# Kernel optimization log

Measured on AMD Instinct MI355X. Metric: run time of the kernel, lower is better.

The kernel has to match this reference:

```python
import jax, jax.numpy as jnp
import numpy as np

N, E = 8192, 65536
IN_C, OUT_C, EF = 64, 16, 8
L1, L2 = 48, 32  # in - floor((in-out)/3), in - floor(2*(in-out)/3)


def setup_inputs() -> dict:
    key = jax.random.key(0)
    ks = jax.random.split(key, 10)
    rn = lambda k, shape, s: jax.random.normal(k, shape, dtype=jnp.float32) * s
    return {
        "x": jax.random.normal(ks[0], (N, IN_C), dtype=jnp.float32),
        "edge_index": jax.random.randint(ks[1], (2, E), 0, N, dtype=jnp.int32),
        "edge_attr": jax.random.normal(ks[2], (E, EF), dtype=jnp.float32),
        "nn1_w": rn(ks[3], (EF, IN_C * L1), 0.05),
        "nn1_b": jnp.zeros((IN_C * L1,), jnp.float32),
        "root1": rn(ks[4], (IN_C, L1), 0.1),
        "bias1": jnp.zeros((L1,), jnp.float32),
        "nn2_w": rn(ks[5], (EF, L1 * L2), 0.05),
        "nn2_b": jnp.zeros((L1 * L2,), jnp.float32),
        "root2": rn(ks[6], (L1, L2), 0.1),
        "bias2": jnp.zeros((L2,), jnp.float32),
        "mu_w": rn(ks[7], (L2, OUT_C), 0.1),
        "mu_b": jnp.zeros((OUT_C,), jnp.float32),
        "ls_w": rn(ks[8], (L2, OUT_C), 0.1),
        "ls_b": jnp.zeros((OUT_C,), jnp.float32),
    }


def _nnconv(x, src, dst, edge_attr, nn_w, nn_b, root, bias, c_in, c_out):
    # edge MLP -> per-edge weight matrices [E, c_in, c_out]
    w = (edge_attr @ nn_w + nn_b).reshape(-1, c_in, c_out)
    msg = jnp.einsum('ei,eio->eo', x[src], w)  # gather + per-edge matvec
    agg = jax.ops.segment_sum(msg, dst, num_segments=x.shape[0])  # sum aggregation
    return agg + x @ root + bias  # root transform + bias


def _gcn(x, src, dst, w, b):
    n = x.shape[0]
    # degree over target nodes, including self-loop (edge_weight = 1)
    deg = jax.ops.segment_sum(jnp.ones_like(src, jnp.float32), dst, num_segments=n) + 1.0
    dinv = jax.lax.rsqrt(deg)
    h = x @ w
    norm = dinv[src] * dinv[dst]  # [E]
    agg = jax.ops.segment_sum(h[src] * norm[:, None], dst, num_segments=n)
    return agg + h * (1.0 / deg)[:, None] + b  # self-loop contribution: deg_i^{-1}


def reference(x, edge_index, edge_attr, nn1_w, nn1_b, root1, bias1,
              nn2_w, nn2_b, root2, bias2, mu_w, mu_b, ls_w, ls_b):
    src, dst = edge_index[0], edge_index[1]
    h = jax.nn.relu(_nnconv(x, src, dst, edge_attr, nn1_w, nn1_b, root1, bias1, IN_C, L1))
    h = jax.nn.relu(_nnconv(h, src, dst, edge_attr, nn2_w, nn2_b, root2, bias2, L1, L2))
    return (_gcn(h, src, dst, mu_w, mu_b), _gcn(h, src, dst, ls_w, ls_b))
```

## Files before the change

kernel.cpp:

```cpp
#include <hip/hip_runtime.h>

#define NN 8192
#define EE 65536
#define MAXDEG 32
#define ZS1 652
#define ZS2 492
#define WS1 68
#define WS2 100
#define U1_OFF 5216
#define U2_OFF 3936


__global__ __launch_bounds__(256) void k_zero(int* __restrict__ cnt,
                                              int* __restrict__ ssrcb,
                                              float* __restrict__ seab) {
    int n = blockIdx.x * 256 + threadIdx.x;
    cnt[n] = 0;
    ssrcb[n * MAXDEG] = 0;
    float4* p = (float4*)(seab + (size_t)n * MAXDEG * 8);
    p[0] = make_float4(0.f, 0.f, 0.f, 0.f);
    p[1] = make_float4(0.f, 0.f, 0.f, 0.f);
}

__global__ __launch_bounds__(256) void k_bucket(const int* __restrict__ ei,
                                                const float* __restrict__ ea,
                                                const float* __restrict__ nn1_w,
                                                const float* __restrict__ nn1_b,
                                                const float* __restrict__ root1,
                                                const float* __restrict__ nn2_w,
                                                const float* __restrict__ nn2_b,
                                                const float* __restrict__ root2,
                                                int* __restrict__ cnt,
                                                int* __restrict__ ssrcb,
                                                float* __restrict__ seab,
                                                float* __restrict__ WtT1,
                                                float* __restrict__ WtT2) {
    int e = blockIdx.x * 256 + threadIdx.x;
    if (e < 48 * 640) {
        int col = e / 640, k = e - col * 640;
        float v = (k < 512) ? nn1_w[k * 48 + col]
                : (k < 576) ? nn1_b[(k - 512) * 48 + col]
                            : root1[(k - 576) * 48 + col];
        WtT1[e] = v;
    } else if (e < 48 * 640 + 32 * 480) {
        int r = e - 48 * 640;
        int col = r / 480, k = r - col * 480;
        float v = (k < 384) ? nn2_w[k * 32 + col]
                : (k < 432) ? nn2_b[(k - 384) * 32 + col]
                            : root2[(k - 432) * 32 + col];
        WtT2[r] = v;
    }
    if (e >= EE) return;
    int s = ei[e], d = ei[EE + e];
    int pos = atomicAdd(&cnt[d], 1);
    if (pos < MAXDEG) {
        int slot = d * MAXDEG + pos;
        ssrcb[slot] = s;
        const float4* a = (const float4*)(ea + (size_t)e * 8);
        float4* bp = (float4*)(seab + (size_t)slot * 8);
        bp[0] = a[0];
        bp[1] = a[1];
    }
}

__global__ __launch_bounds__(256) void k_L1(const int* __restrict__ cnt,
                                            const int* __restrict__ ssrcb,
                                            const float* __restrict__ seab,
                                            const float* __restrict__ x,
                                            const float* __restrict__ WtT1,
                                            const float* __restrict__ bias1,
                                            float* __restrict__ h1) {
    __shared__ __align__(16) float smem[U1_OFF + 48 * WS1];
    float* Zt = smem;
    float* U  = smem + U1_OFF;
    const int n0 = blockIdx.x * 8;
    {
        const int wv = threadIdx.x >> 6;
        const int i = threadIdx.x & 63;
        const int nnA = wv * 2, nnB = nnA + 1;
        const int rsA = (n0 + nnA) * MAXDEG;
        const int rsB = (n0 + nnB) * MAXDEG;
        float xselfA = x[(size_t)(n0 + nnA) * 64 + i];
        float xselfB = x[(size_t)(n0 + nnB) * 64 + i];
        int dA = cnt[n0 + nnA]; if (dA > MAXDEG) dA = MAXDEG;
        int dB = cnt[n0 + nnB]; if (dB > MAXDEG) dB = MAXDEG;
        const int eA = rsA + dA, eB = rsB + dB;
        int jA = rsA, jB = rsB;
        float aA[8] = {0, 0, 0, 0, 0, 0, 0, 0}, sA = 0.f;
        float aB[8] = {0, 0, 0, 0, 0, 0, 0, 0}, sB = 0.f;
        while (jA < eA || jB < eB) {
            int cjA[8], cjB[8];
#pragma unroll
            for (int p = 0; p < 8; p++) {
                int ja = jA + p; cjA[p] = (ja < eA) ? ja : rsA;
                int jb = jB + p; cjB[p] = (jb < eB) ? jb : rsB;
            }
            int sjA[8], sjB[8];
#pragma unroll
            for (int p = 0; p < 8; p++) { sjA[p] = ssrcb[cjA[p]]; sjB[p] = ssrcb[cjB[p]]; }
            float xvA[8], xvB[8];
#pragma unroll
            for (int p = 0; p < 8; p++) {
                xvA[p] = x[(size_t)sjA[p] * 64 + i];
                xvB[p] = x[(size_t)sjB[p] * 64 + i];
            }
#pragma unroll
            for (int p = 0; p < 8; p++) {
                {
                    const float4* q4 = (const float4*)(seab + (size_t)cjA[p] * 8);
                    float4 e0 = q4[0], e1 = q4[1];
                    float xx = (jA + p < eA) ? xvA[p] : 0.f;
                    aA[0] += e0.x * xx; aA[1] += e0.y * xx; aA[2] += e0.z * xx; aA[3] += e0.w * xx;
                    aA[4] += e1.x * xx; aA[5] += e1.y * xx; aA[6] += e1.z * xx; aA[7] += e1.w * xx;
                    sA += xx;
                }
                {
                    const float4* q4 = (const float4*)(seab + (size_t)cjB[p] * 8);
                    float4 e0 = q4[0], e1 = q4[1];
                    float xx = (jB + p < eB) ? xvB[p] : 0.f;
                    aB[0] += e0.x * xx; aB[1] += e0.y * xx; aB[2] += e0.z * xx; aB[3] += e0.w * xx;
                    aB[4] += e1.x * xx; aB[5] += e1.y * xx; aB[6] += e1.z * xx; aB[7] += e1.w * xx;
                    sB += xx;
                }
            }
            jA += 8; jB += 8;
        }
        float* zrA = Zt + nnA * ZS1;
        float* zrB = Zt + nnB * ZS1;
#pragma unroll
        for (int f = 0; f < 8; f++) { zrA[f * 64 + i] = aA[f]; zrB[f * 64 + i] = aB[f]; }
        zrA[512 + i] = sA; zrB[512 + i] = sB;
        zrA[576 + i] = xselfA;
        zrB[576 + i] = xselfB;
    }
    const int o  = threadIdx.x & 15;
    const int q  = (threadIdx.x >> 4) & 1;
    const int ks = threadIdx.x >> 5;
    const int xsw = (o & 7) << 2;
    const int g0 = threadIdx.x, g1 = threadIdx.x + 256, g2 = threadIdx.x + 512;
    const int c0_ = g0 >> 4, k0_ = (g0 & 15) << 2;
    const int c1_ = g1 >> 4, k1_ = (g1 & 15) << 2;
    const int c2_ = g2 >> 4, k2_ = (g2 & 15) << 2;
    const int sa0 = c0_ * WS1 + (k0_ ^ ((c0_ & 7) << 2));
    const int sa1 = c1_ * WS1 + (k1_ ^ ((c1_ & 7) << 2));
    const int sa2 = c2_ * WS1 + (k2_ ^ ((c2_ & 7) << 2));
    const float* gp0 = WtT1 + c0_ * 640 + k0_;
    const float* gp1 = WtT1 + c1_ * 640 + k1_;
    const float* gp2 = WtT1 + c2_ * 640 + k2_;
    float acc[4][3];
#pragma unroll
    for (int m = 0; m < 4; m++)
#pragma unroll
        for (int cc = 0; cc < 3; cc++) acc[m][cc] = 0.f;
    float4 r0 = *(const float4*)gp0;
    float4 r1 = *(const float4*)gp1;
    float4 r2 = *(const float4*)gp2;
    for (int c = 0; c < 10; ++c) {
        __syncthreads();
        *(float4*)&U[sa0] = r0;
        *(float4*)&U[sa1] = r1;
        *(float4*)&U[sa2] = r2;
        __syncthreads();
        if (c < 9) {
            r0 = *(const float4*)(gp0 + (c + 1) * 64);
            r1 = *(const float4*)(gp1 + (c + 1) * 64);
            r2 = *(const float4*)(gp2 + (c + 1) * 64);
        }
#pragma unroll
        for (int kk = 0; kk < 8; kk += 4) {
            const int kl = ks * 8 + kk;
            const int kx = kl ^ xsw;
            const int kg = c * 64 + kl;
            float4 w0 = *(const float4*)&U[o * WS1 + kx];
            float4 w1 = *(const float4*)&U[(o + 16) * WS1 + kx];
            float4 w2 = *(const float4*)&U[(o + 32) * WS1 + kx];
#pragma unroll
            for (int m = 0; m < 4; m++) {
                float4 z = *(const float4*)&Zt[(q * 4 + m) * ZS1 + kg];
                acc[m][0] += z.x * w0.x; acc[m][1] += z.x * w1.x; acc[m][2] += z.x * w2.x;
                acc[m][0] += z.y * w0.y; acc[m][1] += z.y * w1.y; acc[m][2] += z.y * w2.y;
                acc[m][0] += z.z * w0.z; acc[m][1] += z.z * w1.z; acc[m][2] += z.z * w2.z;
                acc[m][0] += z.w * w0.w; acc[m][1] += z.w * w1.w; acc[m][2] += z.w * w2.w;
            }
        }
    }
    __syncthreads();
#pragma unroll
    for (int m = 0; m < 4; m++) {
        U[(ks * 8 + q * 4 + m) * 48 + o]      = acc[m][0];
        U[(ks * 8 + q * 4 + m) * 48 + o + 16] = acc[m][1];
        U[(ks * 8 + q * 4 + m) * 48 + o + 32] = acc[m][2];
    }
    __syncthreads();
    for (int r = threadIdx.x; r < 8 * 48; r += 256) {
        int nn = r / 48, oc = r - nn * 48;
        float v = bias1[oc];
#pragma unroll
        for (int k = 0; k < 8; k++) v += U[(k * 8 + nn) * 48 + oc];
        h1[(size_t)(n0 + nn) * 48 + oc] = v > 0.f ? v : 0.f;
    }
}

__global__ __launch_bounds__(256) void k_L2(const int* __restrict__ cnt,
                                            const int* __restrict__ ssrcb,
                                            const float* __restrict__ seab,
                                            const float* __restrict__ h1,
                                            const float* __restrict__ WtT2,
                                            const float* __restrict__ bias2,
                                            const float* __restrict__ mu_w,
                                            const float* __restrict__ mu_b,
                                            const float* __restrict__ ls_w,
                                            const float* __restrict__ ls_b,
                                            float* __restrict__ hmu,
                                            float* __restrict__ hls,
                                            float* __restrict__ dinv,
                                            float* __restrict__ out) {
    __shared__ __align__(16) float smem[U2_OFF + 32 * WS2];
    float* Zt = smem;
    float* U  = smem + U2_OFF;
    const int n0 = blockIdx.x * 8;
    {
        const int wv = threadIdx.x >> 6;
        const int i = threadIdx.x & 63;
        if (i < 48) {
            const int nnA = wv * 2, nnB = nnA + 1;
            const int rsA = (n0 + nnA) * MAXDEG;
            const int rsB = (n0 + nnB) * MAXDEG;
            float hselfA = h1[(size_t)(n0 + nnA) * 48 + i];
            float hselfB = h1[(size_t)(n0 + nnB) * 48 + i];
            int dA = cnt[n0 + nnA]; if (dA > MAXDEG) dA = MAXDEG;
            int dB = cnt[n0 + nnB]; if (dB > MAXDEG) dB = MAXDEG;
            const int eA = rsA + dA, eB = rsB + dB;
            int jA = rsA, jB = rsB;
            float aA[8] = {0, 0, 0, 0, 0, 0, 0, 0}, sA = 0.f;
            float aB[8] = {0, 0, 0, 0, 0, 0, 0, 0}, sB = 0.f;
            while (jA < eA || jB < eB) {
                int cjA[8], cjB[8];
#pragma unroll
                for (int p = 0; p < 8; p++) {
                    int ja = jA + p; cjA[p] = (ja < eA) ? ja : rsA;
                    int jb = jB + p; cjB[p] = (jb < eB) ? jb : rsB;
                }
                int sjA[8], sjB[8];
#pragma unroll
                for (int p = 0; p < 8; p++) { sjA[p] = ssrcb[cjA[p]]; sjB[p] = ssrcb[cjB[p]]; }
                float hvA[8], hvB[8];
#pragma unroll
                for (int p = 0; p < 8; p++) {
                    hvA[p] = h1[(size_t)sjA[p] * 48 + i];
                    hvB[p] = h1[(size_t)sjB[p] * 48 + i];
                }
#pragma unroll
                for (int p = 0; p < 8; p++) {
                    {
                        const float4* q4 = (const float4*)(seab + (size_t)cjA[p] * 8);
                        float4 e0 = q4[0], e1 = q4[1];
                        float xx = (jA + p < eA) ? hvA[p] : 0.f;
                        aA[0] += e0.x * xx; aA[1] += e0.y * xx; aA[2] += e0.z * xx; aA[3] += e0.w * xx;
                        aA[4] += e1.x * xx; aA[5] += e1.y * xx; aA[6] += e1.z * xx; aA[7] += e1.w * xx;
                        sA += xx;
                    }
                    {
                        const float4* q4 = (const float4*)(seab + (size_t)cjB[p] * 8);
                        float4 e0 = q4[0], e1 = q4[1];
                        float xx = (jB + p < eB) ? hvB[p] : 0.f;
                        aB[0] += e0.x * xx; aB[1] += e0.y * xx; aB[2] += e0.z * xx; aB[3] += e0.w * xx;
                        aB[4] += e1.x * xx; aB[5] += e1.y * xx; aB[6] += e1.z * xx; aB[7] += e1.w * xx;
                        sB += xx;
                    }
                }
                jA += 8; jB += 8;
            }
            float* zrA = Zt + nnA * ZS2;
            float* zrB = Zt + nnB * ZS2;
#pragma unroll
            for (int f = 0; f < 8; f++) { zrA[f * 48 + i] = aA[f]; zrB[f * 48 + i] = aB[f]; }
            zrA[384 + i] = sA; zrB[384 + i] = sB;
            zrA[432 + i] = hselfA;
            zrB[432 + i] = hselfB;
        }
    }
    const int o  = threadIdx.x & 15;
    const int q  = (threadIdx.x >> 4) & 1;
    const int ks = threadIdx.x >> 5;
    const int xsw = (o & 7) << 2;
    const int g0 = threadIdx.x, g1 = threadIdx.x + 256, g2 = threadIdx.x + 512;
    const int c0_ = g0 / 24, k0_ = (g0 - c0_ * 24) << 2;
    const int c1_ = g1 / 24, k1_ = (g1 - c1_ * 24) << 2;
    const int c2_ = g2 / 24, k2_ = (g2 - c2_ * 24) << 2;
    const int sa0 = c0_ * WS2 + (k0_ ^ ((c0_ & 7) << 2));
    const int sa1 = c1_ * WS2 + (k1_ ^ ((c1_ & 7) << 2));
    const int sa2 = c2_ * WS2 + (k2_ ^ ((c2_ & 7) << 2));
    const float* gp0 = WtT2 + c0_ * 480 + k0_;
    const float* gp1 = WtT2 + c1_ * 480 + k1_;
    const float* gp2 = WtT2 + c2_ * 480 + k2_;
    float acc[4][2];
#pragma unroll
    for (int m = 0; m < 4; m++) { acc[m][0] = 0.f; acc[m][1] = 0.f; }
    float4 r0 = *(const float4*)gp0;
    float4 r1 = *(const float4*)gp1;
    float4 r2 = *(const float4*)gp2;
    for (int c = 0; c < 5; ++c) {
        __syncthreads();
        *(float4*)&U[sa0] = r0;
        *(float4*)&U[sa1] = r1;
        *(float4*)&U[sa2] = r2;
        __syncthreads();
        if (c < 4) {
            r0 = *(const float4*)(gp0 + (c + 1) * 96);
            r1 = *(const float4*)(gp1 + (c + 1) * 96);
            r2 = *(const float4*)(gp2 + (c + 1) * 96);
        }
#pragma unroll
        for (int kk = 0; kk < 12; kk += 4) {
            const int kl = ks * 12 + kk;
            const int kx = kl ^ xsw;
            const int kg = c * 96 + kl;
            float4 w0 = *(const float4*)&U[o * WS2 + kx];
            float4 w1 = *(const float4*)&U[(o + 16) * WS2 + kx];
#pragma unroll
            for (int m = 0; m < 4; m++) {
                float4 z = *(const float4*)&Zt[(q * 4 + m) * ZS2 + kg];
                acc[m][0] += z.x * w0.x; acc[m][1] += z.x * w1.x;
                acc[m][0] += z.y * w0.y; acc[m][1] += z.y * w1.y;
                acc[m][0] += z.z * w0.z; acc[m][1] += z.z * w1.z;
                acc[m][0] += z.w * w0.w; acc[m][1] += z.w * w1.w;
            }
        }
    }
    __syncthreads();
#pragma unroll
    for (int m = 0; m < 4; m++) {
        U[(ks * 8 + q * 4 + m) * 32 + o]      = acc[m][0];
        U[(ks * 8 + q * 4 + m) * 32 + o + 16] = acc[m][1];
    }
    __syncthreads();
    {
        int nn = threadIdx.x >> 5, oc = threadIdx.x & 31;
        float v = bias2[oc];
#pragma unroll
        for (int k = 0; k < 8; k++) v += U[(k * 8 + nn) * 32 + oc];
        U[2048 + nn * 33 + oc] = v > 0.f ? v : 0.f;
    }
    __syncthreads();
    if (threadIdx.x < 128) {
        const int oc = threadIdx.x & 15;
        const int nn = threadIdx.x >> 4;
        const int gn = n0 + nn;
        float am = 0.f, al = 0.f;
#pragma unroll
        for (int i = 0; i < 32; i++) {
            float hv = U[2048 + nn * 33 + i];
            am += hv * mu_w[i * 16 + oc];
            al += hv * ls_w[i * 16 + oc];
        }
        float d = (float)cnt[gn] + 1.0f;
        float di = rsqrtf(d);
        if (oc == 0) dinv[gn] = di;
        hmu[(size_t)gn * 16 + oc] = am;
        hls[(size_t)gn * 16 + oc] = al;
        out[(size_t)gn * 16 + oc] = am / d + mu_b[oc];
        out[(size_t)NN * 16 + (size_t)gn * 16 + oc] = al / d + ls_b[oc];
    }
}

__global__ __launch_bounds__(256) void k_gcn(const int* __restrict__ cnt,
                                             const int* __restrict__ ssrcb,
                                             const float* __restrict__ hmu,
                                             const float* __restrict__ hls,
                                             const float* __restrict__ dinv,
                                             float* __restrict__ out) {
    const int wave = threadIdx.x >> 6;
    const int lane = threadIdx.x & 63;
    const int o = lane & 15, p = lane >> 4;
    const int d = blockIdx.x * 4 + wave;
    int deg = cnt[d]; if (deg > MAXDEG) deg = MAXDEG;
    const int rs = d * MAXDEG, re = rs + deg;
    float am = 0.f, al = 0.f;
    for (int j = rs + p; j < re; j += 8) {
        int jb = j + 4;
        int sa = ssrcb[j];
        int sb = ssrcb[jb < re ? jb : rs];
        float da_ = dinv[sa], db_ = dinv[sb];
        float ma = hmu[(size_t)sa * 16 + o], la = hls[(size_t)sa * 16 + o];
        float mb = hmu[(size_t)sb * 16 + o], lb = hls[(size_t)sb * 16 + o];
        am += ma * da_; al += la * da_;
        if (jb < re) { am += mb * db_; al += lb * db_; }
    }
    am += __shfl_xor(am, 16); al += __shfl_xor(al, 16);
    am += __shfl_xor(am, 32); al += __shfl_xor(al, 32);
    if (p == 0) {
        float dd = dinv[d];
        out[(size_t)d * 16 + o] += am * dd;
        out[(size_t)NN * 16 + (size_t)d * 16 + o] += al * dd;
    }
}

extern "C" void kernel_launch(void* const* d_in, const int* in_sizes, int n_in,
                              void* d_out, int out_size, void* d_ws, size_t ws_size,
                              hipStream_t stream) {
    const float* x     = (const float*)d_in[0];
    const int*   ei    = (const int*)d_in[1];
    const float* ea    = (const float*)d_in[2];
    const float* nn1_w = (const float*)d_in[3];
    const float* nn1_b = (const float*)d_in[4];
    const float* root1 = (const float*)d_in[5];
    const float* bias1 = (const float*)d_in[6];
    const float* nn2_w = (const float*)d_in[7];
    const float* nn2_b = (const float*)d_in[8];
    const float* root2 = (const float*)d_in[9];
    const float* bias2 = (const float*)d_in[10];
    const float* mu_w  = (const float*)d_in[11];
    const float* mu_b  = (const float*)d_in[12];
    const float* ls_w  = (const float*)d_in[13];
    const float* ls_b  = (const float*)d_in[14];
    float* out = (float*)d_out;

    float* W     = (float*)d_ws;
    float* WtT1  = W;
    float* WtT2  = WtT1 + 30720;
    float* seab  = WtT2 + 15360;
    float* h1    = seab + NN * MAXDEG * 8;
    float* hmu   = h1 + 393216;
    float* hls   = hmu + 131072;
    float* dinv  = hls + 131072;
    int* cnt     = (int*)(dinv + 8192);
    int* ssrcb   = cnt + 8192;

    k_zero<<<dim3(NN / 256), dim3(256), 0, stream>>>(cnt, ssrcb, seab);
    k_bucket<<<dim3(EE / 256), dim3(256), 0, stream>>>(ei, ea,
                                                       nn1_w, nn1_b, root1,
                                                       nn2_w, nn2_b, root2,
                                                       cnt, ssrcb, seab, WtT1, WtT2);
    k_L1<<<dim3(NN / 8), dim3(256), 0, stream>>>(cnt, ssrcb, seab, x,
                                                 WtT1, bias1, h1);
    k_L2<<<dim3(NN / 8), dim3(256), 0, stream>>>(cnt, ssrcb, seab, h1,
                                                 WtT2, bias2,
                                                 mu_w, mu_b, ls_w, ls_b,
                                                 hmu, hls, dinv, out);
    k_gcn<<<dim3(NN / 4), dim3(256), 0, stream>>>(cnt, ssrcb,
                                                  hmu, hls, dinv, out);
}
```

Before: 145.5 us.

## Fuse GCN aggregation into layer-2 kernel via push-style atomic scatter

Removes the separate GCN gather kernel. k_bucket now also builds an out-edge bucket list (dstb) with per-source counts. The end of k_L2 then pushes each node's normalized mu/logstd projections to its destinations with float atomicAdd into the output, and k_zero now also clears the output buffer. This drops one launch and the hmu/hls/dinv intermediate round-trip to memory. In exchange it adds many scattered global atomics, an extra atomic per edge during bucketing, and non-deterministic summation order.

```diff
diff --git a/kernel.cpp b/kernel.cpp
--- a/kernel.cpp
+++ b/kernel.cpp
@@ -11,15 +11,22 @@
 #define U2_OFF 3936
 
 
-__global__ __launch_bounds__(256) void k_zero(int* __restrict__ cnt,
+__global__ __launch_bounds__(256) void k_zero(float* __restrict__ out,
+                                              int* __restrict__ cntreg,
                                               int* __restrict__ ssrcb,
                                               float* __restrict__ seab) {
-    int n = blockIdx.x * 256 + threadIdx.x;
-    cnt[n] = 0;
-    ssrcb[n * MAXDEG] = 0;
-    float4* p = (float4*)(seab + (size_t)n * MAXDEG * 8);
-    p[0] = make_float4(0.f, 0.f, 0.f, 0.f);
-    p[1] = make_float4(0.f, 0.f, 0.f, 0.f);
+    int i = blockIdx.x * 256 + threadIdx.x;
+    if (i < 65536) {
+        ((float4*)out)[i] = make_float4(0.f, 0.f, 0.f, 0.f);
+    } else {
+        ((int4*)cntreg)[i - 65536] = make_int4(0, 0, 0, 0);
+    }
+    if (i < NN) {
+        ssrcb[i * MAXDEG] = 0;
+        float4* p = (float4*)(seab + (size_t)i * MAXDEG * 8);
+        p[0] = make_float4(0.f, 0.f, 0.f, 0.f);
+        p[1] = make_float4(0.f, 0.f, 0.f, 0.f);
+    }
 }
 
 __global__ __launch_bounds__(256) void k_bucket(const int* __restrict__ ei,
@@ -31,7 +38,9 @@
                                                 const float* __restrict__ nn2_b,
                                                 const float* __restrict__ root2,
                                                 int* __restrict__ cnt,
+                                                int* __restrict__ cnt_src,
                                                 int* __restrict__ ssrcb,
+                                                int* __restrict__ dstb,
                                                 float* __restrict__ seab,
                                                 float* __restrict__ WtT1,
                                                 float* __restrict__ WtT2) {
@@ -61,6 +70,8 @@
         bp[0] = a[0];
         bp[1] = a[1];
     }
+    int pos2 = atomicAdd(&cnt_src[s], 1);
+    if (pos2 < MAXDEG) dstb[s * MAXDEG + pos2] = d;
 }
 
 __global__ __launch_bounds__(256) void k_L1(const int* __restrict__ cnt,
@@ -202,7 +213,9 @@
 }
 
 __global__ __launch_bounds__(256) void k_L2(const int* __restrict__ cnt,
+                                            const int* __restrict__ cnt_src,
                                             const int* __restrict__ ssrcb,
+                                            const int* __restrict__ dstb,
                                             const float* __restrict__ seab,
                                             const float* __restrict__ h1,
                                             const float* __restrict__ WtT2,
@@ -211,9 +224,6 @@
                                             const float* __restrict__ mu_b,
                                             const float* __restrict__ ls_w,
                                             const float* __restrict__ ls_b,
-                                            float* __restrict__ hmu,
-                                            float* __restrict__ hls,
-                                            float* __restrict__ dinv,
                                             float* __restrict__ out) {
     __shared__ __align__(16) float smem[U2_OFF + 32 * WS2];
     float* Zt = smem;
@@ -356,43 +366,17 @@
         }
         float d = (float)cnt[gn] + 1.0f;
         float di = rsqrtf(d);
-        if (oc == 0) dinv[gn] = di;
-        hmu[(size_t)gn * 16 + oc] = am;
-        hls[(size_t)gn * 16 + oc] = al;
-        out[(size_t)gn * 16 + oc] = am / d + mu_b[oc];
-        out[(size_t)NN * 16 + (size_t)gn * 16 + oc] = al / d + ls_b[oc];
-    }
-}
-
-__global__ __launch_bounds__(256) void k_gcn(const int* __restrict__ cnt,
-                                             const int* __restrict__ ssrcb,
-                                             const float* __restrict__ hmu,
-                                             const float* __restrict__ hls,
-                                             const float* __restrict__ dinv,
-                                             float* __restrict__ out) {
-    const int wave = threadIdx.x >> 6;
-    const int lane = threadIdx.x & 63;
-    const int o = lane & 15, p = lane >> 4;
-    const int d = blockIdx.x * 4 + wave;
-    int deg = cnt[d]; if (deg > MAXDEG) deg = MAXDEG;
-    const int rs = d * MAXDEG, re = rs + deg;
-    float am = 0.f, al = 0.f;
-    for (int j = rs + p; j < re; j += 8) {
-        int jb = j + 4;
-        int sa = ssrcb[j];
-        int sb = ssrcb[jb < re ? jb : rs];
-        float da_ = dinv[sa], db_ = dinv[sb];
-        float ma = hmu[(size_t)sa * 16 + o], la = hls[(size_t)sa * 16 + o];
-        float mb = hmu[(size_t)sb * 16 + o], lb = hls[(size_t)sb * 16 + o];
-        am += ma * da_; al += la * da_;
-        if (jb < re) { am += mb * db_; al += lb * db_; }
-    }
-    am += __shfl_xor(am, 16); al += __shfl_xor(al, 16);
-    am += __shfl_xor(am, 32); al += __shfl_xor(al, 32);
-    if (p == 0) {
-        float dd = dinv[d];
-        out[(size_t)d * 16 + o] += am * dd;
-        out[(size_t)NN * 16 + (size_t)d * 16 + o] += al * dd;
+        atomicAdd(out + (size_t)gn * 16 + oc, am / d + mu_b[oc]);
+        atomicAdd(out + (size_t)NN * 16 + (size_t)gn * 16 + oc, al / d + ls_b[oc]);
+        float wm = am * di, wl = al * di;
+        int odeg = cnt_src[gn]; if (odeg > MAXDEG) odeg = MAXDEG;
+        const int rs = gn * MAXDEG;
+        for (int j = 0; j < odeg; ++j) {
+            int d2 = dstb[rs + j];
+            float dd = rsqrtf((float)cnt[d2] + 1.0f);
+            atomicAdd(out + (size_t)d2 * 16 + oc, wm * dd);
+            atomicAdd(out + (size_t)NN * 16 + (size_t)d2 * 16 + oc, wl * dd);
+        }
     }
 }
 
@@ -420,24 +404,21 @@
     float* WtT1  = W;
     float* WtT2  = WtT1 + 30720;
     float* seab  = WtT2 + 15360;
-    float* h1    = seab + NN * MAXDEG * 8;
-    float* hmu   = h1 + 393216;
-    float* hls   = hmu + 131072;
-    float* dinv  = hls + 131072;
-    int* cnt     = (int*)(dinv + 8192);
-    int* ssrcb   = cnt + 8192;
-
-    k_zero<<<dim3(NN / 256), dim3(256), 0, stream>>>(cnt, ssrcb, seab);
+    float* h1    = seab + (size_t)NN * MAXDEG * 8;
+    int* cnt     = (int*)(h1 + 393216);
+    int* cnt_src = cnt + 8192;
+    int* ssrcb   = cnt_src + 8192;
+    int* dstb    = ssrcb + NN * MAXDEG;
+
+    k_zero<<<dim3(272), dim3(256), 0, stream>>>(out, cnt, ssrcb, seab);
     k_bucket<<<dim3(EE / 256), dim3(256), 0, stream>>>(ei, ea,
                                                        nn1_w, nn1_b, root1,
                                                        nn2_w, nn2_b, root2,
-                                                       cnt, ssrcb, seab, WtT1, WtT2);
+                                                       cnt, cnt_src, ssrcb, dstb,
+                                                       seab, WtT1, WtT2);
     k_L1<<<dim3(NN / 8), dim3(256), 0, stream>>>(cnt, ssrcb, seab, x,
                                                  WtT1, bias1, h1);
-    k_L2<<<dim3(NN / 8), dim3(256), 0, stream>>>(cnt, ssrcb, seab, h1,
-                                                 WtT2, bias2,
-                                                 mu_w, mu_b, ls_w, ls_b,
-                                                 hmu, hls, dinv, out);
-    k_gcn<<<dim3(NN / 4), dim3(256), 0, stream>>>(cnt, ssrcb,
-                                                  hmu, hls, dinv, out);
+    k_L2<<<dim3(NN / 8), dim3(256), 0, stream>>>(cnt, cnt_src, ssrcb, dstb,
+                                                 seab, h1, WtT2, bias2,
+                                                 mu_w, mu_b, ls_w, ls_b, out);
 }
```

After: 149.3 us. 1.03x slower.
